# Performance work log

Measured on AMD Instinct MI355X. Metric: run time of the kernel, lower is better.

Reference implementation:

```python
import jax, jax.numpy as jnp
import numpy as np

B, T, C, H = 8, 2048, 768, 64  # batch, seq_len, embedding_dim, head_size


def setup_inputs() -> dict:
    key = jax.random.key(0)
    k1, k2, k3, k4 = jax.random.split(key, 4)
    x = jax.random.normal(k1, (B, T, C), dtype=jnp.float32)
    attention_mask = jnp.ones((B, T), dtype=jnp.float32)
    # nn.Linear(C, H, bias=False) weights stored pre-transposed as (C, H)
    scale = 0.02
    Wq = jax.random.normal(k2, (C, H), dtype=jnp.float32) * scale
    Wk = jax.random.normal(k3, (C, H), dtype=jnp.float32) * scale
    Wv = jax.random.normal(k4, (C, H), dtype=jnp.float32) * scale
    return {"x": x, "attention_mask": attention_mask, "Wq": Wq, "Wk": Wk, "Wv": Wv}


def reference(x, attention_mask, Wq, Wk, Wv):
    # x: [B,T,C]; attention_mask: [B,T] (multiplied per query row)
    head_size = Wq.shape[-1]
    q = x @ Wq  # [B,T,H]
    k = x @ Wk  # [B,T,H]
    v = x @ Wv  # [B,T,H]
    inv_sqrt_h = jnp.asarray(1.0 / np.sqrt(head_size), x.dtype)
    s = jnp.einsum('bqh,bkh->bqk', q, k) * inv_sqrt_h  # [B,T,T]
    # attention_mask.unsqueeze(2) * qK ; masked_fill(qK == 0, -inf)
    s = attention_mask[:, :, None] * s
    s = jnp.where(s == 0, -jnp.inf, s)
    # causal tril mask
    seq = x.shape[1]
    tril = jnp.tril(jnp.ones((seq, seq), dtype=bool))
    s = jnp.where(tril[None, :, :], s, -jnp.inf)
    p = jax.nn.softmax(s, axis=-1)
    # dropout p=0.0 -> identity; nan cleanup (fully-masked rows)
    p = jnp.where(jnp.isnan(p), jnp.asarray(0.0, p.dtype), p)
    out = jnp.einsum('bqk,bkh->bqh', p, v)  # [B,T,H]
    return out
```

## Files before the change

kernel.cpp:

```cpp
#include <hip/hip_runtime.h>
#include <hip/hip_bf16.h>

#define B_ 8
#define T_ 2048
#define C_ 768
#define H_ 64
#define BT_ (B_*T_)

typedef __attribute__((ext_vector_type(8))) short bf16x8;
typedef __attribute__((ext_vector_type(4))) float f32x4;

__device__ __forceinline__ unsigned short f2bf(float x) {
    __hip_bfloat16 h = __float2bfloat16(x);
    return __builtin_bit_cast(unsigned short, h);
}

__device__ __forceinline__ bf16x8 cvt8(float4 a, float4 b) {
    bf16x8 r;
    r[0] = (short)f2bf(a.x); r[1] = (short)f2bf(a.y);
    r[2] = (short)f2bf(a.z); r[3] = (short)f2bf(a.w);
    r[4] = (short)f2bf(b.x); r[5] = (short)f2bf(b.y);
    r[6] = (short)f2bf(b.z); r[7] = (short)f2bf(b.w);
    return r;
}

__global__ __launch_bounds__(256) void wprep(
    const float* __restrict__ Wq, const float* __restrict__ Wk,
    const float* __restrict__ Wv, unsigned short* __restrict__ WTf)
{
    __shared__ float tile[32][68];
    const int bid = blockIdx.x;
    const int m = bid / 24, gc = bid % 24;
    const float* __restrict__ W = (m == 0) ? Wq : (m == 1) ? Wk : Wv;
    const int t = threadIdx.x;
    {
        const int r = t >> 3, c0 = (t & 7) * 8;
        float4 a = *(const float4*)(W + (size_t)(gc * 32 + r) * H_ + c0);
        float4 b = *(const float4*)(W + (size_t)(gc * 32 + r) * H_ + c0 + 4);
        *(float4*)&tile[r][c0]     = a;
        *(float4*)&tile[r][c0 + 4] = b;
    }
    __syncthreads();
    const int fl = t >> 6, lane = t & 63;
    const int q16 = lane & 15, quad = lane >> 4;
    const int f = m * 4 + fl;
    ushort4 u0, u1;
    u0.x = f2bf(tile[quad * 8 + 0][fl * 16 + q16]);
    u0.y = f2bf(tile[quad * 8 + 1][fl * 16 + q16]);
    u0.z = f2bf(tile[quad * 8 + 2][fl * 16 + q16]);
    u0.w = f2bf(tile[quad * 8 + 3][fl * 16 + q16]);
    u1.x = f2bf(tile[quad * 8 + 4][fl * 16 + q16]);
    u1.y = f2bf(tile[quad * 8 + 5][fl * 16 + q16]);
    u1.z = f2bf(tile[quad * 8 + 6][fl * 16 + q16]);
    u1.w = f2bf(tile[quad * 8 + 7][fl * 16 + q16]);
    unsigned short* __restrict__ dst = WTf + ((size_t)(gc * 12 + f) * 64 + lane) * 8;
    *(ushort4*)(dst)     = u0;
    *(ushort4*)(dst + 4) = u1;
}

__global__ __launch_bounds__(256) void qkv_kernel(
    const float* __restrict__ x, const unsigned short* __restrict__ WTf,
    unsigned short* __restrict__ qF, unsigned short* __restrict__ kF,
    unsigned short* __restrict__ vF)
{
    __shared__ __align__(16) unsigned short xS[16 * 772];
    const int tid  = threadIdx.x;
    const int w    = tid >> 6;
    const int lane = tid & 63;
    const int q16  = lane & 15, quad = lane >> 4;
    const int rowBase = blockIdx.x << 4;

    {
        const int r = tid >> 4, l = tid & 15;
        const float* __restrict__ xrow = x + (size_t)(rowBase + r) * C_;
        #pragma unroll
        for (int i = 0; i < 6; i++) {
            const int j = i * 16 + l;
            float4 a = *(const float4*)(xrow + j * 8);
            float4 b = *(const float4*)(xrow + j * 8 + 4);
            *(bf16x8*)&xS[(size_t)r * 772 + j * 8] = cvt8(a, b);
        }
    }
    __syncthreads();

    const int f0 = w * 3;
    const unsigned short* __restrict__ xrowS = xS + q16 * 772 + quad * 8;
    f32x4 acc[3] = {};
    #pragma unroll
    for (int c = 0; c < 24; c++) {
        const unsigned short* __restrict__ wpc =
            WTf + ((size_t)(c * 12 + f0)) * 512 + lane * 8;
        bf16x8 xf = *(const bf16x8*)(xrowS + c * 32);
        bf16x8 w0 = *(const bf16x8*)(wpc);
        bf16x8 w1 = *(const bf16x8*)(wpc + 512);
        bf16x8 w2 = *(const bf16x8*)(wpc + 1024);
        acc[0] = __builtin_amdgcn_mfma_f32_16x16x32_bf16(w0, xf, acc[0], 0, 0, 0);
        acc[1] = __builtin_amdgcn_mfma_f32_16x16x32_bf16(w1, xf, acc[1], 0, 0, 0);
        acc[2] = __builtin_amdgcn_mfma_f32_16x16x32_bf16(w2, xf, acc[2], 0, 0, 0);
    }

    const size_t gt = (size_t)(rowBase >> 4);
    #pragma unroll
    for (int j = 0; j < 3; j++) {
        const int f = f0 + j;
        if (f < 8) {
            ushort4 u;
            u.x = f2bf(acc[j][0]); u.y = f2bf(acc[j][1]);
            u.z = f2bf(acc[j][2]); u.w = f2bf(acc[j][3]);
            const int n4 = f & 3;
            const int qp = (2 * n4 + (quad >> 1)) & 3;
            const int j0 = (quad & 1) * 4;
            unsigned short* __restrict__ dst = (f < 4) ? qF : kF;
            *(ushort4*)(dst + ((gt * 2 + (n4 >> 1)) * 64 + q16 + 16 * qp) * 8 + j0) = u;
        } else {
            const size_t g32 = gt >> 1;
            const int qv = ((int)gt & 1) * 2 + (q16 >> 3);
            const int jv = q16 & 7;
            #pragma unroll
            for (int r = 0; r < 4; r++)
                vF[((g32 * 4 + (f - 8)) * 64 + quad * 4 + r + 16 * qv) * 8 + jv] =
                    f2bf(acc[j][r]);
        }
    }
}

__global__ __launch_bounds__(256) void attn_kernel(
    const unsigned short* __restrict__ qF, const unsigned short* __restrict__ kF,
    const unsigned short* __restrict__ vF, const float* __restrict__ mask,
    float* __restrict__ out)
{
    __shared__ __align__(16) unsigned short pS[4][16][88];
    __shared__ float oS[3][64][17];

    const int tid  = threadIdx.x;
    const int w    = tid >> 6;
    const int lane = tid & 63;
    const int q16  = lane & 15;
    const int quad = lane >> 4;
    const int bid  = blockIdx.x;
    const int b    = bid & 7;
    const int g    = 63 - (bid >> 3);
    const int qtA  = 2 * g, qtB = 2 * g + 1;
    const int qrowA = (qtA << 4) + q16;
    const int qrowB = qrowA + 16;

    const size_t qbaseA = ((size_t)(b * 128 + qtA) * 2) * 512 + lane * 8;
    const size_t qbaseB = ((size_t)(b * 128 + qtB) * 2) * 512 + lane * 8;
    bf16x8 qfA0 = *(const bf16x8*)(qF + qbaseA);
    bf16x8 qfA1 = *(const bf16x8*)(qF + qbaseA + 512);
    bf16x8 qfB0 = *(const bf16x8*)(qF + qbaseB);
    bf16x8 qfB1 = *(const bf16x8*)(qF + qbaseB + 512);
    const float mrowA  = mask[b * T_ + qrowA];
    const float mrowB  = mask[b * T_ + qrowB];
    const float maskvA = mrowA * 0.125f * 1.44269504f;
    const float maskvB = mrowB * 0.125f * 1.44269504f;

    f32x4 oA[4] = {}, oB[4] = {};
    float lA = 0.f, lB = 0.f;

    const int niter = ((qtB << 4) + 16 + 63) >> 6;
    const int dt    = niter - 1;

    bf16x8 kf[8], vf[8];
    auto loadK = [&](int kt_) {
        #pragma unroll
        for (int sub = 0; sub < 4; sub++) {
            const unsigned short* kp = kF + ((size_t)(b * 128 + kt_ * 4 + sub) * 2) * 512 + lane * 8;
            kf[2 * sub]     = *(const bf16x8*)(kp);
            kf[2 * sub + 1] = *(const bf16x8*)(kp + 512);
        }
    };
    auto loadV = [&](int kt_) {
        #pragma unroll
        for (int ht = 0; ht < 4; ht++) {
            const unsigned short* vp = vF + ((size_t)(b * 64 + kt_ * 2) * 4 + ht) * 512 + lane * 8;
            vf[2 * ht]     = *(const bf16x8*)(vp);
            vf[2 * ht + 1] = *(const bf16x8*)(vp + 4 * 512);
        }
    };

    if (w < niter) { loadK(w); loadV(w); }

    for (int kt = w; kt < niter; kt += 4) {
        const int kbase = kt << 6;
        const bool more = (kt + 4 < niter);

        f32x4 saA[4] = {}, saB[4] = {};
        #pragma unroll
        for (int sub = 0; sub < 4; sub++) {
            saA[sub] = __builtin_amdgcn_mfma_f32_16x16x32_bf16(kf[2 * sub],     qfA0, saA[sub], 0, 0, 0);
            saA[sub] = __builtin_amdgcn_mfma_f32_16x16x32_bf16(kf[2 * sub + 1], qfA1, saA[sub], 0, 0, 0);
            saB[sub] = __builtin_amdgcn_mfma_f32_16x16x32_bf16(kf[2 * sub],     qfB0, saB[sub], 0, 0, 0);
            saB[sub] = __builtin_amdgcn_mfma_f32_16x16x32_bf16(kf[2 * sub + 1], qfB1, saB[sub], 0, 0, 0);
        }
        if (more) loadK(kt + 4);

        {
            float p[16];
            if (kt != dt) {
                #pragma unroll
                for (int e = 0; e < 16; e++)
                    p[e] = __builtin_amdgcn_exp2f(saA[e >> 2][e & 3] * maskvA);
            } else {
                #pragma unroll
                for (int sub = 0; sub < 4; sub++)
                    #pragma unroll
                    for (int r = 0; r < 4; r++) {
                        int kidx = kbase + sub * 16 + quad * 4 + r;
                        float sv = saA[sub][r] * maskvA;
                        sv = (kidx > qrowA) ? -__builtin_inff() : sv;
                        p[sub * 4 + r] = __builtin_amdgcn_exp2f(sv);
                    }
            }
            lA += (((p[0] + p[1]) + (p[2] + p[3])) + ((p[4] + p[5]) + (p[6] + p[7])))
                + (((p[8] + p[9]) + (p[10] + p[11])) + ((p[12] + p[13]) + (p[14] + p[15])));
            #pragma unroll
            for (int sub = 0; sub < 4; sub++) {
                unsigned int lo = (unsigned int)f2bf(p[sub * 4 + 0]) | ((unsigned int)f2bf(p[sub * 4 + 1]) << 16);
                unsigned int hi = (unsigned int)f2bf(p[sub * 4 + 2]) | ((unsigned int)f2bf(p[sub * 4 + 3]) << 16);
                *(uint2*)&pS[w][q16][sub * 16 + quad * 4] = make_uint2(lo, hi);
            }
            bf16x8 pf0 = *(const bf16x8*)&pS[w][q16][quad * 8];
            bf16x8 pf1 = *(const bf16x8*)&pS[w][q16][32 + quad * 8];
            #pragma unroll
            for (int ht = 0; ht < 4; ht++) {
                oA[ht] = __builtin_amdgcn_mfma_f32_16x16x32_bf16(vf[2 * ht],     pf0, oA[ht], 0, 0, 0);
                oA[ht] = __builtin_amdgcn_mfma_f32_16x16x32_bf16(vf[2 * ht + 1], pf1, oA[ht], 0, 0, 0);
            }
        }

        {
            float p[16];
            if (kt != dt) {
                #pragma unroll
                for (int e = 0; e < 16; e++)
                    p[e] = __builtin_amdgcn_exp2f(saB[e >> 2][e & 3] * maskvB);
            } else {
                #pragma unroll
                for (int sub = 0; sub < 4; sub++)
                    #pragma unroll
                    for (int r = 0; r < 4; r++) {
                        int kidx = kbase + sub * 16 + quad * 4 + r;
                        float sv = saB[sub][r] * maskvB;
                        sv = (kidx > qrowB) ? -__builtin_inff() : sv;
                        p[sub * 4 + r] = __builtin_amdgcn_exp2f(sv);
                    }
            }
            lB += (((p[0] + p[1]) + (p[2] + p[3])) + ((p[4] + p[5]) + (p[6] + p[7])))
                + (((p[8] + p[9]) + (p[10] + p[11])) + ((p[12] + p[13]) + (p[14] + p[15])));
            #pragma unroll
            for (int sub = 0; sub < 4; sub++) {
                unsigned int lo = (unsigned int)f2bf(p[sub * 4 + 0]) | ((unsigned int)f2bf(p[sub * 4 + 1]) << 16);
                unsigned int hi = (unsigned int)f2bf(p[sub * 4 + 2]) | ((unsigned int)f2bf(p[sub * 4 + 3]) << 16);
                *(uint2*)&pS[w][q16][sub * 16 + quad * 4] = make_uint2(lo, hi);
            }
            bf16x8 pf0 = *(const bf16x8*)&pS[w][q16][quad * 8];
            bf16x8 pf1 = *(const bf16x8*)&pS[w][q16][32 + quad * 8];
            #pragma unroll
            for (int ht = 0; ht < 4; ht++) {
                oB[ht] = __builtin_amdgcn_mfma_f32_16x16x32_bf16(vf[2 * ht],     pf0, oB[ht], 0, 0, 0);
                oB[ht] = __builtin_amdgcn_mfma_f32_16x16x32_bf16(vf[2 * ht + 1], pf1, oB[ht], 0, 0, 0);
            }
        }
        if (more) loadV(kt + 4);
    }

    lA += __shfl_xor(lA, 16); lA += __shfl_xor(lA, 32);
    lB += __shfl_xor(lB, 16); lB += __shfl_xor(lB, 32);

    if (w > 0) {
        #pragma unroll
        for (int ht = 0; ht < 4; ht++)
            #pragma unroll
            for (int r = 0; r < 4; r++) oS[w - 1][lane][ht * 4 + r] = oA[ht][r];
        oS[w - 1][lane][16] = lA;
    }
    __syncthreads();
    if (w == 0) {
        #pragma unroll
        for (int j = 0; j < 3; j++) {
            #pragma unroll
            for (int ht = 0; ht < 4; ht++)
                #pragma unroll
                for (int r = 0; r < 4; r++) oA[ht][r] += oS[j][lane][ht * 4 + r];
            lA += oS[j][lane][16];
        }
        const float invl = (mrowA != 0.f && lA > 0.f) ? (1.f / lA) : 0.f;
        #pragma unroll
        for (int ht = 0; ht < 4; ht++) {
            float4 ov = make_float4(oA[ht][0] * invl, oA[ht][1] * invl,
                                    oA[ht][2] * invl, oA[ht][3] * invl);
            *(float4*)(out + ((size_t)(b * T_) + qrowA) * H_ + ht * 16 + quad * 4) = ov;
        }
    }
    __syncthreads();

    if (w > 0) {
        #pragma unroll
        for (int ht = 0; ht < 4; ht++)
            #pragma unroll
            for (int r = 0; r < 4; r++) oS[w - 1][lane][ht * 4 + r] = oB[ht][r];
        oS[w - 1][lane][16] = lB;
    }
    __syncthreads();
    if (w == 0) {
        #pragma unroll
        for (int j = 0; j < 3; j++) {
            #pragma unroll
            for (int ht = 0; ht < 4; ht++)
                #pragma unroll
                for (int r = 0; r < 4; r++) oB[ht][r] += oS[j][lane][ht * 4 + r];
            lB += oS[j][lane][16];
        }
        const float invl = (mrowB != 0.f && lB > 0.f) ? (1.f / lB) : 0.f;
        #pragma unroll
        for (int ht = 0; ht < 4; ht++) {
            float4 ov = make_float4(oB[ht][0] * invl, oB[ht][1] * invl,
                                    oB[ht][2] * invl, oB[ht][3] * invl);
            *(float4*)(out + ((size_t)(b * T_) + qrowB) * H_ + ht * 16 + quad * 4) = ov;
        }
    }
}

extern "C" void kernel_launch(void* const* d_in, const int* in_sizes, int n_in,
                              void* d_out, int out_size, void* d_ws, size_t ws_size,
                              hipStream_t stream) {
    const float* x    = (const float*)d_in[0];
    const float* mask = (const float*)d_in[1];
    const float* Wq   = (const float*)d_in[2];
    const float* Wk   = (const float*)d_in[3];
    const float* Wv   = (const float*)d_in[4];
    float* out = (float*)d_out;

    unsigned short* qf = (unsigned short*)d_ws;
    unsigned short* kf = qf + (size_t)BT_ * H_;
    unsigned short* vf = kf + (size_t)BT_ * H_;
    unsigned short* wt = vf + (size_t)BT_ * H_;

    wprep<<<72, 256, 0, stream>>>(Wq, Wk, Wv, wt);
    qkv_kernel<<<BT_ / 16, 256, 0, stream>>>(x, wt, qf, kf, vf);
    attn_kernel<<<B_ * (T_ / 32), 256, 0, stream>>>(qf, kf, vf, mask, out);
}
```

Baseline: 114.6 us.

## Keep projection weights in registers and process four row tiles per QKV block

The QKV projection kernel now runs 12 waves per block, one per output 16-column fragment. Each wave loads its full slice of weights into registers once and reuses it across four 16-row tiles of x, which are staged in LDS together. Four independent accumulators are summed at the end to break the MFMA dependency chain. This cuts repeated global weight loads and raises MFMA ILP, at the cost of heavy register pressure (24 bf16x8 weight vectors per lane), more LDS per block, and four times fewer blocks.

After: 140.8 us. 1.23x slower.

```diff
diff --git a/kernel.cpp b/kernel.cpp
--- a/kernel.cpp
+++ b/kernel.cpp
@@ -58,59 +58,62 @@
     *(ushort4*)(dst + 4) = u1;
 }
 
-__global__ __launch_bounds__(256) void qkv_kernel(
+__global__ __launch_bounds__(768, 3) void qkv_kernel(
     const float* __restrict__ x, const unsigned short* __restrict__ WTf,
     unsigned short* __restrict__ qF, unsigned short* __restrict__ kF,
     unsigned short* __restrict__ vF)
 {
-    __shared__ __align__(16) unsigned short xS[16 * 772];
+    __shared__ __align__(16) unsigned short xS[4][16 * 772];
     const int tid  = threadIdx.x;
     const int w    = tid >> 6;
     const int lane = tid & 63;
     const int q16  = lane & 15, quad = lane >> 4;
-    const int rowBase = blockIdx.x << 4;
-
-    {
-        const int r = tid >> 4, l = tid & 15;
-        const float* __restrict__ xrow = x + (size_t)(rowBase + r) * C_;
+    const int rowBase = blockIdx.x << 6;
+
+    bf16x8 wreg[24];
+    #pragma unroll
+    for (int c = 0; c < 24; c++)
+        wreg[c] = *(const bf16x8*)(WTf + ((size_t)(c * 12 + w)) * 512 + lane * 8);
+
+    #pragma unroll 2
+    for (int pass = 0; pass < 8; pass++) {
+        const int gl  = pass * 768 + tid;
+        const int row = gl / 96, g = gl - row * 96;
+        const int tt  = row >> 4, r = row & 15;
+        const float* __restrict__ xrow = x + (size_t)(rowBase + row) * C_;
+        float4 a = *(const float4*)(xrow + g * 8);
+        float4 b = *(const float4*)(xrow + g * 8 + 4);
+        *(bf16x8*)&xS[tt][(size_t)r * 772 + g * 8] = cvt8(a, b);
+    }
+    __syncthreads();
+
+    const size_t gt0 = (size_t)(rowBase >> 4);
+    #pragma unroll
+    for (int tt = 0; tt < 4; tt++) {
+        const unsigned short* __restrict__ xrowS = xS[tt] + q16 * 772 + quad * 8;
+        f32x4 a0 = {}, a1 = {}, a2 = {}, a3 = {};
         #pragma unroll
         for (int i = 0; i < 6; i++) {
-            const int j = i * 16 + l;
-            float4 a = *(const float4*)(xrow + j * 8);
-            float4 b = *(const float4*)(xrow + j * 8 + 4);
-            *(bf16x8*)&xS[(size_t)r * 772 + j * 8] = cvt8(a, b);
-        }
-    }
-    __syncthreads();
-
-    const int f0 = w * 3;
-    const unsigned short* __restrict__ xrowS = xS + q16 * 772 + quad * 8;
-    f32x4 acc[3] = {};
-    #pragma unroll
-    for (int c = 0; c < 24; c++) {
-        const unsigned short* __restrict__ wpc =
-            WTf + ((size_t)(c * 12 + f0)) * 512 + lane * 8;
-        bf16x8 xf = *(const bf16x8*)(xrowS + c * 32);
-        bf16x8 w0 = *(const bf16x8*)(wpc);
-        bf16x8 w1 = *(const bf16x8*)(wpc + 512);
-        bf16x8 w2 = *(const bf16x8*)(wpc + 1024);
-        acc[0] = __builtin_amdgcn_mfma_f32_16x16x32_bf16(w0, xf, acc[0], 0, 0, 0);
-        acc[1] = __builtin_amdgcn_mfma_f32_16x16x32_bf16(w1, xf, acc[1], 0, 0, 0);
-        acc[2] = __builtin_amdgcn_mfma_f32_16x16x32_bf16(w2, xf, acc[2], 0, 0, 0);
-    }
-
-    const size_t gt = (size_t)(rowBase >> 4);
-    #pragma unroll
-    for (int j = 0; j < 3; j++) {
-        const int f = f0 + j;
-        if (f < 8) {
+            a0 = __builtin_amdgcn_mfma_f32_16x16x32_bf16(
+                     wreg[4 * i + 0], *(const bf16x8*)(xrowS + (4 * i + 0) * 32), a0, 0, 0, 0);
+            a1 = __builtin_amdgcn_mfma_f32_16x16x32_bf16(
+                     wreg[4 * i + 1], *(const bf16x8*)(xrowS + (4 * i + 1) * 32), a1, 0, 0, 0);
+            a2 = __builtin_amdgcn_mfma_f32_16x16x32_bf16(
+                     wreg[4 * i + 2], *(const bf16x8*)(xrowS + (4 * i + 2) * 32), a2, 0, 0, 0);
+            a3 = __builtin_amdgcn_mfma_f32_16x16x32_bf16(
+                     wreg[4 * i + 3], *(const bf16x8*)(xrowS + (4 * i + 3) * 32), a3, 0, 0, 0);
+        }
+        f32x4 acc = (a0 + a1) + (a2 + a3);
+
+        const size_t gt = gt0 + tt;
+        if (w < 8) {
             ushort4 u;
-            u.x = f2bf(acc[j][0]); u.y = f2bf(acc[j][1]);
-            u.z = f2bf(acc[j][2]); u.w = f2bf(acc[j][3]);
-            const int n4 = f & 3;
+            u.x = f2bf(acc[0]); u.y = f2bf(acc[1]);
+            u.z = f2bf(acc[2]); u.w = f2bf(acc[3]);
+            const int n4 = w & 3;
             const int qp = (2 * n4 + (quad >> 1)) & 3;
             const int j0 = (quad & 1) * 4;
-            unsigned short* __restrict__ dst = (f < 4) ? qF : kF;
+            unsigned short* __restrict__ dst = (w < 4) ? qF : kF;
             *(ushort4*)(dst + ((gt * 2 + (n4 >> 1)) * 64 + q16 + 16 * qp) * 8 + j0) = u;
         } else {
             const size_t g32 = gt >> 1;
@@ -118,8 +121,8 @@
             const int jv = q16 & 7;
             #pragma unroll
             for (int r = 0; r < 4; r++)
-                vF[((g32 * 4 + (f - 8)) * 64 + quad * 4 + r + 16 * qv) * 8 + jv] =
-                    f2bf(acc[j][r]);
+                vF[((g32 * 4 + (w - 8)) * 64 + quad * 4 + r + 16 * qv) * 8 + jv] =
+                    f2bf(acc[r]);
         }
     }
 }
@@ -338,6 +341,6 @@
     unsigned short* wt = vf + (size_t)BT_ * H_;
 
     wprep<<<72, 256, 0, stream>>>(Wq, Wk, Wv, wt);
-    qkv_kernel<<<BT_ / 16, 256, 0, stream>>>(x, wt, qf, kf, vf);
+    qkv_kernel<<<BT_ / 64, 768, 0, stream>>>(x, wt, qf, kf, vf);
     attn_kernel<<<B_ * (T_ / 32), 256, 0, stream>>>(qf, kf, vf, mask, out);
 }
```
